# Kernel tuning notes

Measured on AMD Instinct MI355X. Metric: run time of the kernel, lower is better.

The kernel has to match this reference:

```python
import jax, jax.numpy as jnp
import numpy as np

B, G, CE, D, L, H, DH, M, KQ = 4, 64, 384, 512, 8, 16, 32, 2048, 16
NJ, NB = 163, 11
DET_THRESH = 0.3
PATCH = 14.0
EPS = 1e-8


def _ln(x, g, b):
    mu = x.mean(-1, keepdims=True)
    v = x.var(-1, keepdims=True)
    return (x - mu) * jax.lax.rsqrt(v + 1e-5) * g + b


def setup_inputs():
    key = jax.random.key(0)
    ks = iter(jax.random.split(key, 64))
    def n(sh, s=0.02):
        return (jax.random.normal(next(ks), sh) * s).astype(jnp.float32)
    inp = {}
    inp['feat'] = jax.random.normal(next(ks), (B, G, G, CE), dtype=jnp.float32)
    inp['scores'] = jax.random.uniform(next(ks), (B, G, G), dtype=jnp.float32)
    inp['K_cam'] = jnp.tile(jnp.array([[1000., 0., 448.], [0., 1000., 448.], [0., 0., 1.]], dtype=jnp.float32), (B, 1, 1))
    inp['pos_emb'] = n((G * G, D), 1.0)
    inp['Wtok'] = n((CE, D)); inp['btok'] = jnp.zeros((D,), jnp.float32)
    for nm in ['Wq', 'Wk', 'Wv', 'Wo']:
        inp[nm] = n((L, D, D))
    inp['g1'] = jnp.ones((L, D), jnp.float32); inp['b1n'] = jnp.zeros((L, D), jnp.float32)
    inp['W1'] = n((L, D, M)); inp['bf1'] = jnp.zeros((L, M), jnp.float32)
    inp['W2'] = n((L, M, D)); inp['bf2'] = jnp.zeros((L, D), jnp.float32)
    inp['g2'] = jnp.ones((L, D), jnp.float32); inp['b2n'] = jnp.zeros((L, D), jnp.float32)
    inp['offW1'] = n((D, D)); inp['offb1'] = jnp.zeros((D,), jnp.float32)
    inp['offW2'] = n((D, 2)); inp['offb2'] = jnp.zeros((2,), jnp.float32)
    inp['dW1'] = n((D, D)); inp['db1'] = jnp.zeros((D,), jnp.float32)
    inp['dW2'] = n((D, 1)); inp['db2'] = jnp.zeros((1,), jnp.float32)
    inp['sW1'] = n((D, D)); inp['sb1'] = jnp.zeros((D,), jnp.float32)
    inp['sW2'] = n((D, NB)); inp['sb2'] = jnp.zeros((NB,), jnp.float32)
    inp['pW1'] = n((D + NJ * 6, D)); inp['pb1'] = jnp.zeros((D,), jnp.float32)
    inp['pW2'] = n((D, NJ * 6)); inp['pb2'] = jnp.zeros((NJ * 6,), jnp.float32)
    # identity-like 6D init pose per joint: eye(3)[:, :2].flatten() = [1,0,0,1,0,0]
    inp['init_body_pose'] = jnp.tile(jnp.array([1., 0., 0., 1., 0., 0.], dtype=jnp.float32), NJ)
    inp['useful_rotmat'] = (jax.random.uniform(next(ks), (NJ,)) < 0.66).astype(jnp.float32)
    return inp


def reference(feat, scores, K_cam, pos_emb, Wtok, btok,
              Wq, Wk, Wv, Wo, g1, b1n, W1, bf1, W2, bf2, g2, b2n,
              offW1, offb1, offW2, offb2, dW1, db1, dW2, db2,
              sW1, sb1, sW2, sb2, pW1, pb1, pW2, pb2,
              init_body_pose, useful_rotmat):
    # --- NMS via 3x3 max-pool (stride 1, same padding) + threshold ---
    sm = jax.lax.reduce_window(scores, -jnp.inf, jax.lax.max, (1, 3, 3), (1, 1, 1), 'SAME')
    sc = scores * (sm == scores).astype(scores.dtype)
    flat = sc.reshape(B, G * G)
    vals, idx = jax.lax.top_k(flat, KQ)                 # padded ragged detections
    mask = (vals >= DET_THRESH).astype(feat.dtype)      # [B,KQ] validity mask
    row = idx // G
    col = idx % G
    # --- token projection + 2d pos emb, gather queries ---
    dec_emb = feat @ Wtok + btok + pos_emb.reshape(G, G, D)        # [B,G,G,D]
    ctx = dec_emb.reshape(B, G * G, D)                              # context per image
    q = jnp.take_along_axis(ctx, idx[..., None], axis=1)            # [B,KQ,D]
    x = q * mask[..., None]
    scale = DH ** -0.5
    # --- HPH decoder: depth x (prenorm cross-attn to full-image context + FFN) ---
    for l in range(L):
        h = _ln(x, g1[l], b1n[l])
        qh = (h @ Wq[l]).reshape(B, KQ, H, DH)
        kh = (ctx @ Wk[l]).reshape(B, G * G, H, DH)
        vh = (ctx @ Wv[l]).reshape(B, G * G, H, DH)
        att = jax.nn.softmax(jnp.einsum('bqhd,bkhd->bhqk', qh, kh) * scale, axis=-1)
        o = jnp.einsum('bhqk,bkhd->bqhd', att, vh).reshape(B, KQ, H * DH) @ Wo[l]
        x = x + o * mask[..., None]
        h2 = _ln(x, g2[l], b2n[l])
        x = x + (jax.nn.gelu(h2 @ W1[l] + bf1[l]) @ W2[l] + bf2[l]) * mask[..., None]
    y = x.reshape(B * KQ, D)
    m = mask.reshape(B * KQ, 1)
    # --- heads ---
    offset = jax.nn.relu(y @ offW1 + offb1) @ offW2 + offb2          # [N,2]
    loc_coarse = jnp.stack([col.reshape(-1), row.reshape(-1)], -1).astype(y.dtype)
    loc = (loc_coarse + 0.5 + offset) * PATCH
    Kd = jnp.repeat(K_cam, KQ, axis=0)                               # [N,3,3]
    focal = Kd[:, 0, 0]
    d_raw = jax.nn.relu(y @ dW1 + db1) @ dW2 + db2                   # [N,1]
    dist = focal[:, None] / jnp.clip(jnp.exp(d_raw), 1e-5)
    homo = jnp.concatenate([loc, jnp.ones_like(loc[:, :1])], -1)     # [N,3]
    Kinv = jnp.linalg.inv(Kd)
    transl = jnp.einsum('nij,nj->ni', Kinv, homo) * dist             # [N,3]
    shape_ = jax.nn.sigmoid(jax.nn.relu(y @ sW1 + sb1) @ sW2 + sb2)  # [N,11]
    ibp = jnp.broadcast_to(init_body_pose, (B * KQ, NJ * 6))
    rot6d = jax.nn.relu(jnp.concatenate([y, ibp], -1) @ pW1 + pb1) @ pW2 + pb2 + ibp
    # --- special Gram-Schmidt: 6D -> rotation matrices ---
    Mm = rot6d.reshape(-1, NJ, 3, 2)
    u0 = Mm[..., 0]
    u0 = u0 / (jnp.linalg.norm(u0, axis=-1, keepdims=True) + EPS)
    v1 = Mm[..., 1] - jnp.sum(Mm[..., 1] * u0, -1, keepdims=True) * u0
    u1 = v1 / (jnp.linalg.norm(v1, axis=-1, keepdims=True) + EPS)
    u2 = jnp.cross(u0, u1)
    rotmat = jnp.stack([u0, u1, u2], -1)                             # [N,NJ,3,3]
    eye = jnp.eye(3, dtype=rotmat.dtype)
    um = useful_rotmat.reshape(1, NJ, 1, 1)
    rotmat = um * rotmat + (1.0 - um) * eye
    out = jnp.concatenate([loc, offset, dist, transl, shape_, rotmat.reshape(B * KQ, NJ * 9)], -1) * m
    return out
```

## Files before the change

### kernel.cpp

```cpp
#include <hip/hip_runtime.h>

typedef unsigned int uint;
typedef unsigned short u16;

#define BB 4
#define CE 384
#define DD 512
#define LL 8
#define HH 16
#define MM 2048
#define NJ 163
#define TOK 4096
#define BKQ 64
#define QH 256
#define OUTW 1486
#define NROT 978
#define QKSCALE 0.17677669529663687f

typedef __attribute__((ext_vector_type(8))) short short8;
typedef __attribute__((ext_vector_type(4))) float float4v;

static __device__ __forceinline__ u16 f2bf(float f){
  union { float f; uint u; } c; c.f = f;
  uint u = c.u;
  return (u16)((u + 0x7FFFu + ((u >> 16) & 1u)) >> 16);
}
static __device__ __forceinline__ float bf2f(u16 u){
  union { uint u; float f; } c; c.u = ((uint)u) << 16;
  return c.f;
}
static __device__ __forceinline__ float wred_sum(float v){
  for (int o = 32; o; o >>= 1) v += __shfl_xor(v, o, 64);
  return v;
}
static __device__ __forceinline__ void gl16(const void* g, void* l){
  __builtin_amdgcn_global_load_lds((const __attribute__((address_space(1))) void*)g,
                                   (__attribute__((address_space(3))) void*)l, 16, 0, 0);
}

__global__ __launch_bounds__(256) void k_nms_topk(const float* __restrict__ scores,
    int* __restrict__ oidx, float* __restrict__ omask, float* __restrict__ ocol, float* __restrict__ orow)
{
  int b = blockIdx.x, t = threadIdx.x;
  __shared__ float sraw[4096];
  __shared__ float sv[4]; __shared__ int si[4]; __shared__ int swin;
  const float* sp = scores + (size_t)b * 4096;
  for (int i = t; i < 4096; i += 256) sraw[i] = sp[i];
  __syncthreads();
  float v[16];
  #pragma unroll
  for (int j = 0; j < 16; j++){
    int i = t + j*256;
    int r = i >> 6, c = i & 63;
    float mx = -1e30f;
    for (int dr = -1; dr <= 1; dr++){
      int rr = r + dr; if (rr < 0 || rr > 63) continue;
      for (int dc = -1; dc <= 1; dc++){
        int cc = c + dc; if (cc < 0 || cc > 63) continue;
        mx = fmaxf(mx, sraw[rr*64+cc]);
      }
    }
    float s = sraw[i];
    v[j] = (s == mx) ? s : 0.0f;
  }
  int lane = t & 63, wv = t >> 6;
  for (int iter = 0; iter < 16; iter++){
    float best = -1e30f; int bi_ = 1 << 30;
    #pragma unroll
    for (int j = 0; j < 16; j++){
      if (v[j] > best){ best = v[j]; bi_ = t + j*256; }
    }
    #pragma unroll
    for (int o = 32; o; o >>= 1){
      float ov = __shfl_xor(best, o, 64);
      int oi = __shfl_xor(bi_, o, 64);
      if (ov > best || (ov == best && oi < bi_)){ best = ov; bi_ = oi; }
    }
    if (lane == 0){ sv[wv] = best; si[wv] = bi_; }
    __syncthreads();
    if (t == 0){
      float bb = sv[0]; int ii = si[0];
      for (int k = 1; k < 4; k++){
        if (sv[k] > bb || (sv[k] == bb && si[k] < ii)){ bb = sv[k]; ii = si[k]; }
      }
      oidx[b*16+iter] = ii;
      omask[b*16+iter] = (bb >= 0.3f) ? 1.f : 0.f;
      ocol[b*16+iter] = (float)(ii & 63);
      orow[b*16+iter] = (float)(ii >> 6);
      swin = ii;
    }
    __syncthreads();
    int wi = swin;
    if ((wi & 255) == t) v[wi >> 8] = -1e30f;
    __syncthreads();
  }
}

__global__ __launch_bounds__(256) void k_cvt_bf16(const float* __restrict__ in, u16* __restrict__ out, int n4){
  int i = blockIdx.x*256 + threadIdx.x;
  int stride = gridDim.x*256;
  for (int j = i; j < n4; j += stride){
    float4 v = ((const float4*)in)[j];
    ushort4 o;
    o.x = f2bf(v.x); o.y = f2bf(v.y); o.z = f2bf(v.z); o.w = f2bf(v.w);
    ((ushort4*)out)[j] = o;
  }
}

struct PJobs {
  const float* s[24]; u16* d[24];
  int R[24], C[24], t0[25];
  int njobs, ntiles;
};
__global__ __launch_bounds__(256) void k_prep_all(PJobs J,
    const float* __restrict__ pW1, const float* __restrict__ pb1,
    const float* __restrict__ ibp, float* __restrict__ hb4,
    const float* __restrict__ offb1, const float* __restrict__ db1, const float* __restrict__ sb1,
    const float* __restrict__ pb2, float* __restrict__ cvec2)
{
  int bid = blockIdx.x, t = threadIdx.x;
  if (bid < 128){
    int d = bid*4 + (t >> 6);
    int ln = t & 63;
    float acc = 0.f;
    for (int i = ln; i < NJ*6; i += 64) acc += ibp[i] * pW1[(size_t)(DD+i)*DD + d];
    acc = wred_sum(acc);
    if (ln == 0) hb4[1536 + d] = acc + pb1[d];
  } else if (bid == 128){
    for (int i = t; i < 1536; i += 256)
      hb4[i] = (i < 512) ? offb1[i] : (i < 1024 ? db1[i-512] : sb1[i-1024]);
    for (int i = t; i < 1024; i += 256)
      cvec2[i] = (i < NJ*6) ? (pb2[i] + ibp[i]) : 0.f;
  }
  __shared__ float tile[32][33];
  for (int g = bid; g < J.ntiles; g += gridDim.x){
    int j = 0;
    while (g >= J.t0[j+1]) j++;
    int ti = g - J.t0[j];
    int C_ = J.C[j], R_ = J.R[j];
    int tC = (C_ + 31) >> 5;
    int ry = ti / tC, cx = ti - ry*tC;
    int c0 = cx*32, r0 = ry*32;
    int tx = t & 31, ty = t >> 5;
    const float* src = J.s[j]; u16* dst = J.d[j];
    for (int i = 0; i < 32; i += 8){
      float v = 0.f;
      if (c0+tx < C_) v = src[(size_t)(r0+ty+i)*C_ + c0+tx];
      tile[ty+i][tx] = v;
    }
    __syncthreads();
    for (int i = 0; i < 32; i += 8){
      if (c0+ty+i < C_) dst[(size_t)(c0+ty+i)*R_ + r0+tx] = f2bf(tile[tx][ty+i]);
    }
    __syncthreads();
  }
}

__global__ __launch_bounds__(256) void k_wqkvo(const float* __restrict__ wq, const float* __restrict__ wk,
    const float* __restrict__ wv, const float* __restrict__ wo,
    u16* __restrict__ AT, u16* __restrict__ WVOT)
{
  __shared__ __align__(16) u16 As[2560];
  __shared__ __align__(16) u16 Bs[2560];
  int t = threadIdx.x;
  int lane = t & 63, w = t >> 6, lr = lane & 15, lk = lane >> 4;
  float4v acc[4];
  float4v z4 = {0.f,0.f,0.f,0.f};
  acc[0]=z4; acc[1]=z4; acc[2]=z4; acc[3]=z4;
  if (blockIdx.x < 1024){
    int id = blockIdx.x;
    int rt = id & 127, dt = id >> 7;
    int h = rt >> 3, dout0 = (rt & 7)*64, din0 = dt*64;
    int r = t >> 2, c0 = (t & 3)*8;
    {
      float4 u0 = *(const float4*)(wk + (size_t)(dout0+r)*DD + h*32 + c0);
      float4 u1 = *(const float4*)(wk + (size_t)(dout0+r)*DD + h*32 + c0 + 4);
      u16* d = As + r*40 + c0;
      d[0]=f2bf(u0.x); d[1]=f2bf(u0.y); d[2]=f2bf(u0.z); d[3]=f2bf(u0.w);
      d[4]=f2bf(u1.x); d[5]=f2bf(u1.y); d[6]=f2bf(u1.z); d[7]=f2bf(u1.w);
      float4 v0 = *(const float4*)(wq + (size_t)(din0+r)*DD + h*32 + c0);
      float4 v1 = *(const float4*)(wq + (size_t)(din0+r)*DD + h*32 + c0 + 4);
      u16* e = Bs + r*40 + c0;
      e[0]=f2bf(v0.x); e[1]=f2bf(v0.y); e[2]=f2bf(v0.z); e[3]=f2bf(v0.w);
      e[4]=f2bf(v1.x); e[5]=f2bf(v1.y); e[6]=f2bf(v1.z); e[7]=f2bf(v1.w);
    }
    __syncthreads();
    short8 af = *(const short8*)&As[(w*16+lr)*40 + lk*8];
    #pragma unroll
    for (int nf = 0; nf < 4; nf++){
      short8 bf8 = *(const short8*)&Bs[(nf*16+lr)*40 + lk*8];
      acc[nf] = __builtin_amdgcn_mfma_f32_16x16x32_bf16(af, bf8, acc[nf], 0, 0, 0);
    }
    #pragma unroll
    for (int nf = 0; nf < 4; nf++){
      #pragma unroll
      for (int jj = 0; jj < 4; jj++){
        int row = w*16 + lk*4 + jj;
        AT[(size_t)(h*512 + dout0 + row)*DD + din0 + nf*16 + lr] = f2bf(acc[nf][jj]*QKSCALE);
      }
    }
  } else {
    int id = blockIdx.x - 1024;
    int ct = id & 127, dt = id >> 7;
    int h = ct >> 3, Dc0 = (ct & 7)*64, dout0 = dt*64;
    {
      int c = t >> 3, d8 = (t & 7)*8;
      float4 a0 = *(const float4*)(wo + (size_t)(h*32+c)*DD + dout0 + d8);
      float4 a1 = *(const float4*)(wo + (size_t)(h*32+c)*DD + dout0 + d8 + 4);
      As[(d8+0)*40 + c] = f2bf(a0.x);
      As[(d8+1)*40 + c] = f2bf(a0.y);
      As[(d8+2)*40 + c] = f2bf(a0.z);
      As[(d8+3)*40 + c] = f2bf(a0.w);
      As[(d8+4)*40 + c] = f2bf(a1.x);
      As[(d8+5)*40 + c] = f2bf(a1.y);
      As[(d8+6)*40 + c] = f2bf(a1.z);
      As[(d8+7)*40 + c] = f2bf(a1.w);
      int r = t >> 2, c0 = (t & 3)*8;
      float4 v0 = *(const float4*)(wv + (size_t)(Dc0+r)*DD + h*32 + c0);
      float4 v1 = *(const float4*)(wv + (size_t)(Dc0+r)*DD + h*32 + c0 + 4);
      u16* e = Bs + r*40 + c0;
      e[0]=f2bf(v0.x); e[1]=f2bf(v0.y); e[2]=f2bf(v0.z); e[3]=f2bf(v0.w);
      e[4]=f2bf(v1.x); e[5]=f2bf(v1.y); e[6]=f2bf(v1.z); e[7]=f2bf(v1.w);
    }
    __syncthreads();
    short8 af = *(const short8*)&As[(w*16+lr)*40 + lk*8];
    #pragma unroll
    for (int nf = 0; nf < 4; nf++){
      short8 bf8 = *(const short8*)&Bs[(nf*16+lr)*40 + lk*8];
      acc[nf] = __builtin_amdgcn_mfma_f32_16x16x32_bf16(af, bf8, acc[nf], 0, 0, 0);
    }
    #pragma unroll
    for (int nf = 0; nf < 4; nf++){
      #pragma unroll
      for (int jj = 0; jj < 4; jj++){
        int row = w*16 + lk*4 + jj;
        WVOT[(size_t)(dout0 + row)*8192 + h*512 + Dc0 + nf*16 + lr] = f2bf(acc[nf][jj]);
      }
    }
  }
}

__global__ __launch_bounds__(256) void k_red8(const u16* __restrict__ parts, u16* __restrict__ cf){
  int i4 = blockIdx.x*256 + threadIdx.x;
  int elem = i4*4;
  int row = elem >> 13, col = elem & 8191;
  int b = row >> 4, q = row & 15, h = col >> 9, Dc = col & 511;
  const u16* src = parts + ((size_t)b*8)*131072 + (size_t)(q*16+h)*512 + Dc;
  float s0 = 0.f, s1 = 0.f, s2 = 0.f, s3 = 0.f;
  #pragma unroll
  for (int ks = 0; ks < 8; ks++){
    ushort4 g = *(const ushort4*)(src + (size_t)ks*131072);
    s0 += bf2f(g.x); s1 += bf2f(g.y); s2 += bf2f(g.z); s3 += bf2f(g.w);
  }
  ushort4 o;
  o.x = f2bf(s0); o.y = f2bf(s1); o.z = f2bf(s2); o.w = f2bf(s3);
  *(ushort4*)&cf[(size_t)row*8192 + col] = o;
}

__global__ __launch_bounds__(256) void k_gemm_emb(
    const float* __restrict__ feat, const u16* __restrict__ Bt,
    u16* __restrict__ ctx, u16* __restrict__ ctxT,
    const float* __restrict__ ep1, const float* __restrict__ ep2)
{
  __shared__ __align__(16) u16 SM[16640];
  u16* As = SM;
  u16* Bs = SM + 8192;
  int m0 = blockIdx.y*128, n0 = blockIdx.x*128;
  int t = threadIdx.x, lane = t & 63, wave = t >> 6;
  int wr = wave >> 1, wc = wave & 1;
  int lr = lane & 15, lk = lane >> 4;
  int sr8 = t >> 3, sl = t & 7;
  int sw = ((sl ^ (sr8 & 7)) * 8);
  float4v acc[4][4];
  float4v z4 = {0.f, 0.f, 0.f, 0.f};
  #pragma unroll
  for (int i = 0; i < 4; i++)
    #pragma unroll
    for (int j = 0; j < 4; j++) acc[i][j] = z4;
  for (int kt = 0; kt < CE; kt += 64){
    __syncthreads();
    #pragma unroll
    for (int p = 0; p < 8; p++){
      int r = (t >> 4) + p*16, f4 = t & 15;
      float4 v = *(const float4*)&feat[(size_t)(m0+r)*CE + kt + f4*4];
      int dc = ((f4 >> 1) ^ (r & 7))*8 + (f4 & 1)*4;
      ushort4 o; o.x = f2bf(v.x); o.y = f2bf(v.y); o.z = f2bf(v.z); o.w = f2bf(v.w);
      *(ushort4*)&As[r*64 + dc] = o;
    }
    #pragma unroll
    for (int rg = 0; rg < 4; rg++)
      gl16(Bt + (size_t)(n0 + rg*32 + sr8)*CE + kt + sw, Bs + rg*2048 + 8*t);
    __syncthreads();
    #pragma unroll
    for (int s = 0; s < 2; s++){
      int slot = ((s*4 + lk) ^ (lr & 7)) * 8;
      short8 af[4], bfr[4];
      #pragma unroll
      for (int i = 0; i < 4; i++) af[i] = *(const short8*)&As[(wr*64 + i*16 + lr)*64 + slot];
      #pragma unroll
      for (int j = 0; j < 4; j++) bfr[j] = *(const short8*)&Bs[(wc*64 + j*16 + lr)*64 + slot];
      #pragma unroll
      for (int i = 0; i < 4; i++)
        #pragma unroll
        for (int j = 0; j < 4; j++)
          acc[i][j] = __builtin_amdgcn_mfma_f32_16x16x32_bf16(af[i], bfr[j], acc[i][j], 0, 0, 0);
    }
  }
  __syncthreads();
  #pragma unroll
  for (int i = 0; i < 4; i++){
    int rbase = m0 + wr*64 + i*16 + lk*4;
    #pragma unroll
    for (int j = 0; j < 4; j++){
      int cc = n0 + wc*64 + j*16 + lr;
      #pragma unroll
      for (int jj = 0; jj < 4; jj++){
        int rr = rbase + jj;
        float vv = acc[i][j][jj] + ep1[cc] + ep2[(size_t)(rr & 4095)*DD + cc];
        u16 bv = f2bf(vv);
        ctx[(size_t)rr*DD + cc] = bv;
        SM[(cc - n0)*130 + (rr - m0)] = bv;
      }
    }
  }
  __syncthreads();
  int b = m0 >> 12, tok0 = m0 & 4095;
  int tx = t & 63, ty = t >> 6;
  #pragma unroll 4
  for (int it = 0; it < 32; it++){
    int c = ty*32 + it;
    uint vv = *(const uint*)&SM[c*130 + tx*2];
    *(uint*)&ctxT[((size_t)b*DD + n0 + c)*TOK + tok0 + tx*2] = vv;
  }
}

__global__ __launch_bounds__(256) void k_gather2(const u16* __restrict__ ctx, const int* __restrict__ oidx,
    float* __restrict__ x)
{
  int bq = blockIdx.x, t = threadIdx.x;
  int b = bq >> 4, tok = oidx[bq];
  uint v = ((const uint*)(ctx + ((size_t)b*TOK + tok)*DD))[t];
  float2 o; o.x = bf2f((u16)(v & 0xFFFF)); o.y = bf2f((u16)(v >> 16));
  *(float2*)&x[(size_t)bq*DD + t*2] = o;
}

template<int EPI>
__global__ __launch_bounds__(256) void k_gemm_bt64(
    const u16* __restrict__ A, const u16* __restrict__ Bt,
    float* __restrict__ C, u16* __restrict__ Cb,
    int Kslice, int lda, int ldb, int ldc,
    long sA, long sB, long sC, int ksplit)
{
  int bz = blockIdx.z;
  int batch = bz / ksplit, ks = bz - batch*ksplit;
  const u16* Ab = A + (size_t)batch*sA + (size_t)ks*Kslice;
  const u16* Bb = Bt + (size_t)batch*sB + (size_t)ks*Kslice;
  int m0 = blockIdx.y*128, n0 = blockIdx.x*64;
  __shared__ __align__(16) u16 As[128*64];
  __shared__ __align__(16) u16 Bs[64*64];
  int t = threadIdx.x, lane = t & 63, w = t >> 6;
  int lr = lane & 15, lk = lane >> 4;
  int sr8 = t >> 3, sl = t & 7;
  int sw = ((sl ^ (sr8 & 7)) * 8);
  float4v acc[2][4];
  float4v z4 = {0.f,0.f,0.f,0.f};
  #pragma unroll
  for (int i = 0; i < 2; i++)
    #pragma unroll
    for (int j = 0; j < 4; j++) acc[i][j] = z4;

  for (int kt = 0; kt < Kslice; kt += 64){
    __syncthreads();
    #pragma unroll
    for (int rg = 0; rg < 4; rg++)
      gl16(Ab + (size_t)(m0 + rg*32 + sr8)*lda + kt + sw, As + rg*2048 + 8*t);
    #pragma unroll
    for (int rg = 0; rg < 2; rg++)
      gl16(Bb + (size_t)(n0 + rg*32 + sr8)*ldb + kt + sw, Bs + rg*2048 + 8*t);
    __syncthreads();
    #pragma unroll
    for (int s = 0; s < 2; s++){
      int slot = ((s*4 + lk) ^ (lr & 7)) * 8;
      short8 af[2], bfr[4];
      #pragma unroll
      for (int i = 0; i < 2; i++) af[i] = *(const short8*)&As[(w*32 + i*16 + lr)*64 + slot];
      #pragma unroll
      for (int j = 0; j < 4; j++) bfr[j] = *(const short8*)&Bs[(j*16 + lr)*64 + slot];
      #pragma unroll
      for (int i = 0; i < 2; i++)
        #pragma unroll
        for (int j = 0; j < 4; j++)
          acc[i][j] = __builtin_amdgcn_mfma_f32_16x16x32_bf16(af[i], bfr[j], acc[i][j], 0, 0, 0);
    }
  }
  #pragma unroll
  for (int i = 0; i < 2; i++){
    int rbase = m0 + w*32 + i*16 + lk*4;
    #pragma unroll
    for (int j = 0; j < 4; j++){
      int cc = n0 + j*16 + lr;
      #pragma unroll
      for (int jj = 0; jj < 4; jj++){
        int rr = rbase + jj;
        if (EPI == 0) C[(size_t)bz*sC + (size_t)rr*ldc + cc] = acc[i][j][jj];
        else if (EPI == 1) Cb[(size_t)batch*sC + (size_t)rr*ldc + cc] = f2bf(acc[i][j][jj]);
        else Cb[(size_t)bz*sC + (size_t)rr*ldc + cc] = f2bf(acc[i][j][jj]);
      }
    }
  }
}

template<int ACT, int RES, int OUTB, int DOLN, int NG, int HPB, int ZMAP = 0>
__global__ __launch_bounds__(256) void k_mf64(
    const u16* __restrict__ A, const float* __restrict__ xf,
    const float* __restrict__ g, const float* __restrict__ bb,
    const u16* __restrict__ Bt, const float* __restrict__ bias,
    float* __restrict__ C, u16* __restrict__ Cb, u16* __restrict__ Cb2,
    int N, int K, int kper, int ldc, float alpha)
{
  __shared__ __align__(16) u16 Asl[DOLN ? 64*520 : 64*64];
  __shared__ __align__(16) u16 Bs[64*64];
  int t = threadIdx.x, lane = t & 63, w = t >> 6;
  int lr = lane & 15, lk = lane >> 4;
  int n0 = blockIdx.x*64;
  int ks = blockIdx.y, kbeg = ks*kper;
  int sr8 = t >> 3, sl = t & 7;
  int sw = ((sl ^ (sr8 & 7)) * 8);

  if (DOLN){
    for (int rr = 0; rr < 16; rr++){
      int row = w*16 + rr;
      const float* xr = xf + (size_t)row*DD;
      float4 v0 = *(const float4*)(xr + lane*4);
      float4 v1 = *(const float4*)(xr + 256 + lane*4);
      float s = v0.x+v0.y+v0.z+v0.w + v1.x+v1.y+v1.z+v1.w;
      s = wred_sum(s);
      float mu = s * (1.f/DD);
      float d0=v0.x-mu, d1=v0.y-mu, d2=v0.z-mu, d3=v0.w-mu;
      float e0=v1.x-mu, e1=v1.y-mu, e2=v1.z-mu, e3=v1.w-mu;
      float q = d0*d0+d1*d1+d2*d2+d3*d3 + e0*e0+e1*e1+e2*e2+e3*e3;
      q = wred_sum(q);
      float inv = rsqrtf(q * (1.f/DD) + 1e-5f);
      float4 g0 = *(const float4*)(g + lane*4);
      float4 g1 = *(const float4*)(g + 256 + lane*4);
      float4 b0 = *(const float4*)(bb + lane*4);
      float4 b1 = *(const float4*)(bb + 256 + lane*4);
      u16* dst = &Asl[row*520];
      dst[lane*4+0] = f2bf(d0*inv*g0.x + b0.x);
      dst[lane*4+1] = f2bf(d1*inv*g0.y + b0.y);
      dst[lane*4+2] = f2bf(d2*inv*g0.z + b0.z);
      dst[lane*4+3] = f2bf(d3*inv*g0.w + b0.w);
      dst[256+lane*4+0] = f2bf(e0*inv*g1.x + b1.x);
      dst[256+lane*4+1] = f2bf(e1*inv*g1.y + b1.y);
      dst[256+lane*4+2] = f2bf(e2*inv*g1.z + b1.z);
      dst[256+lane*4+3] = f2bf(e3*inv*g1.w + b1.w);
    }
  }

  float4v acc[4];
  float4v z4 = {0.f,0.f,0.f,0.f};
  acc[0]=z4; acc[1]=z4; acc[2]=z4; acc[3]=z4;

  for (int kc = kbeg; kc < kbeg + kper; kc += 64){
    __syncthreads();
    if (!DOLN){
      gl16(A + (size_t)sr8*K + kc + sw,        (u16*)Asl + 8*t);
      gl16(A + (size_t)(32+sr8)*K + kc + sw,   (u16*)Asl + 2048 + 8*t);
    }
    gl16(Bt + (size_t)(n0+sr8)*K + kc + sw,      (u16*)Bs + 8*t);
    gl16(Bt + (size_t)(n0+32+sr8)*K + kc + sw,   (u16*)Bs + 2048 + 8*t);
    __syncthreads();
    #pragma unroll
    for (int s = 0; s < 2; s++){
      int slot = ((s*4 + lk) ^ (lr & 7)) * 8;
      short8 af;
      if (DOLN) af = *(const short8*)&Asl[(w*16+lr)*520 + kc + s*32 + lk*8];
      else      af = *(const short8*)&Asl[(w*16+lr)*64 + slot];
      #pragma unroll
      for (int nf = 0; nf < 4; nf++){
        short8 bf8 = *(const short8*)&Bs[(nf*16+lr)*64 + slot];
        acc[nf] = __builtin_amdgcn_mfma_f32_16x16x32_bf16(af, bf8, acc[nf], 0, 0, 0);
      }
    }
  }
  #pragma unroll
  for (int nf = 0; nf < 4; nf++){
    int col = n0 + nf*16 + lr;
    float bsv = (bias && ks == 0) ? bias[col] : 0.f;
    #pragma unroll
    for (int jj = 0; jj < 4; jj++){
      int row = w*16 + lk*4 + jj;
      float v = acc[nf][jj]*alpha + bsv;
      if (ACT == 1) v = fmaxf(v, 0.f);
      else if (ACT == 2) v = 0.5f*v*(1.f + tanhf(0.7978845608028654f*(v + 0.044715f*v*v*v)));
      if (NG && col >= N) continue;
      if (ZMAP){
        int b_ = row >> 4, q_ = row & 15, h_ = col >> 9, d_ = col & 511;
        Cb[((size_t)b_*QH + (q_ << 4) + h_)*DD + d_] = f2bf(v);
        continue;
      }
      size_t o = (size_t)row*ldc + col;
      if (OUTB == 1) Cb[o] = f2bf(v);
      else if (RES == 0) C[o] = v;
      else atomicAdd(&C[o], v);
      if (HPB && col >= 1536) Cb2[(size_t)row*DD + (col - 1536)] = f2bf(v);
    }
  }
}

__global__ __launch_bounds__(256) void k_softmax(const u16* __restrict__ lg, u16* __restrict__ att){
  int row = blockIdx.x, t = threadIdx.x;
  const uint* p = (const uint*)(lg + (size_t)row*TOK);
  uint pv[8]; float v0[8], v1[8]; float mx = -1e30f;
  #pragma unroll
  for (int i = 0; i < 8; i++){
    pv[i] = p[t + i*256];
    v0[i] = bf2f((u16)(pv[i] & 0xFFFF));
    v1[i] = bf2f((u16)(pv[i] >> 16));
    mx = fmaxf(mx, fmaxf(v0[i], v1[i]));
  }
  int lane = t & 63, w = t >> 6;
  for (int o = 32; o; o >>= 1) mx = fmaxf(mx, __shfl_xor(mx, o, 64));
  __shared__ float sm[4]; __shared__ float ssum[4];
  if (lane == 0) sm[w] = mx;
  __syncthreads();
  mx = fmaxf(fmaxf(sm[0], sm[1]), fmaxf(sm[2], sm[3]));
  float s = 0.f;
  #pragma unroll
  for (int i = 0; i < 8; i++){
    v0[i] = expf(v0[i] - mx); v1[i] = expf(v1[i] - mx);
    s += v0[i] + v1[i];
  }
  s = wred_sum(s);
  if (lane == 0) ssum[w] = s;
  __syncthreads();
  s = ssum[0]+ssum[1]+ssum[2]+ssum[3];
  float inv = 1.f / s;
  uint* q = (uint*)(att + (size_t)row*TOK);
  #pragma unroll
  for (int i = 0; i < 8; i++){
    uint lo = f2bf(v0[i]*inv);
    uint hi = f2bf(v1[i]*inv);
    q[t + i*256] = lo | (hi << 16);
  }
}

__global__ __launch_bounds__(256) void k_final(
    const float* __restrict__ h4, const float* __restrict__ rot6d,
    const float* __restrict__ offW2, const float* __restrict__ offb2,
    const float* __restrict__ dW2, const float* __restrict__ db2,
    const float* __restrict__ sW2, const float* __restrict__ sb2,
    const float* __restrict__ K_cam, const float* __restrict__ useful,
    const float* __restrict__ maskf, const float* __restrict__ colf, const float* __restrict__ rowf,
    float* __restrict__ out)
{
  int bq = blockIdx.x, t = threadIdx.x, b = bq >> 4;
  float po0 = 0.f, po1 = 0.f, pd = 0.f, ps[11];
  #pragma unroll
  for (int j = 0; j < 11; j++) ps[j] = 0.f;
  const float* hrow = h4 + (size_t)bq*2048;
  for (int i = t; i < DD; i += 256){
    float ho = hrow[i];
    float hd = hrow[512 + i];
    float hs = hrow[1024 + i];
    po0 += ho*offW2[i*2]; po1 += ho*offW2[i*2+1];
    pd += hd*dW2[i];
    #pragma unroll
    for (int j = 0; j < 11; j++) ps[j] += hs*sW2[i*11+j];
  }
  __shared__ float sred[4][14];
  __shared__ float sout[14];
  int wv = t >> 6, ln = t & 63;
  float vals[14];
  vals[0] = po0; vals[1] = po1; vals[2] = pd;
  #pragma unroll
  for (int j = 0; j < 11; j++) vals[3+j] = ps[j];
  #pragma unroll
  for (int kk = 0; kk < 14; kk++){
    float r = wred_sum(vals[kk]);
    if (ln == 0) sred[wv][kk] = r;
  }
  __syncthreads();
  if (t < 14) sout[t] = sred[0][t]+sred[1][t]+sred[2][t]+sred[3][t];
  __syncthreads();
  float m = maskf[bq];
  if (t == 0){
    float off0 = sout[0] + offb2[0], off1 = sout[1] + offb2[1];
    float draw = sout[2] + db2[0];
    float l0 = (colf[bq] + 0.5f + off0) * 14.0f;
    float l1 = (rowf[bq] + 0.5f + off1) * 14.0f;
    float fx = K_cam[b*9+0], cx = K_cam[b*9+2], fy = K_cam[b*9+4], cy = K_cam[b*9+5];
    float dist = fx / fmaxf(expf(draw), 1e-5f);
    float tx = (l0 - cx) / fx * dist, ty = (l1 - cy) / fy * dist;
    float* o = out + (size_t)bq*OUTW;
    o[0] = l0*m; o[1] = l1*m; o[2] = off0*m; o[3] = off1*m; o[4] = dist*m;
    o[5] = tx*m; o[6] = ty*m; o[7] = dist*m;
    #pragma unroll
    for (int j = 0; j < 11; j++){ float sp = sout[3+j] + sb2[j]; o[8+j] = m / (1.f + expf(-sp)); }
  }
  if (t < NJ){
    const float* rp = rot6d + (size_t)bq*NROT + t*6;
    float a0 = rp[0], b0 = rp[1], a1 = rp[2], b1 = rp[3], a2 = rp[4], b2 = rp[5];
    float n0 = sqrtf(a0*a0 + a1*a1 + a2*a2);
    float i0 = 1.f / (n0 + 1e-8f);
    float u00 = a0*i0, u01 = a1*i0, u02 = a2*i0;
    float dt = b0*u00 + b1*u01 + b2*u02;
    float v0 = b0 - dt*u00, v1 = b1 - dt*u01, v2 = b2 - dt*u02;
    float n1 = sqrtf(v0*v0 + v1*v1 + v2*v2);
    float i1 = 1.f / (n1 + 1e-8f);
    float u10 = v0*i1, u11 = v1*i1, u12 = v2*i1;
    float u20 = u01*u12 - u02*u11;
    float u21 = u02*u10 - u00*u12;
    float u22 = u00*u11 - u01*u10;
    float um = useful[t], om = 1.f - um;
    float R00 = um*u00 + om, R01 = um*u10,      R02 = um*u20;
    float R10 = um*u01,      R11 = um*u11 + om, R12 = um*u21;
    float R20 = um*u02,      R21 = um*u12,      R22 = um*u22 + om;
    float* o = out + (size_t)bq*OUTW + 19 + t*9;
    o[0] = R00*m; o[1] = R01*m; o[2] = R02*m;
    o[3] = R10*m; o[4] = R11*m; o[5] = R12*m;
    o[6] = R20*m; o[7] = R21*m; o[8] = R22*m;
  }
}

extern "C" void kernel_launch(void* const* d_in, const int* in_sizes, int n_in,
                              void* d_out, int out_size, void* d_ws, size_t ws_size,
                              hipStream_t stream)
{
  const float* feat   = (const float*)d_in[0];
  const float* scores = (const float*)d_in[1];
  const float* K_cam  = (const float*)d_in[2];
  const float* pos_emb= (const float*)d_in[3];
  const float* Wtok   = (const float*)d_in[4];
  const float* btok   = (const float*)d_in[5];
  const float* Wq     = (const float*)d_in[6];
  const float* Wk     = (const float*)d_in[7];
  const float* Wv     = (const float*)d_in[8];
  const float* Wo     = (const float*)d_in[9];
  const float* g1     = (const float*)d_in[10];
  const float* b1n    = (const float*)d_in[11];
  const float* W1     = (const float*)d_in[12];
  const float* bf1    = (const float*)d_in[13];
  const float* W2     = (const float*)d_in[14];
  const float* bf2    = (const float*)d_in[15];
  const float* g2     = (const float*)d_in[16];
  const float* b2n    = (const float*)d_in[17];
  const float* offW1  = (const float*)d_in[18];
  const float* offb1  = (const float*)d_in[19];
  const float* offW2  = (const float*)d_in[20];
  const float* offb2  = (const float*)d_in[21];
  const float* dW1    = (const float*)d_in[22];
  const float* db1    = (const float*)d_in[23];
  const float* dW2    = (const float*)d_in[24];
  const float* db2    = (const float*)d_in[25];
  const float* sW1    = (const float*)d_in[26];
  const float* sb1    = (const float*)d_in[27];
  const float* sW2    = (const float*)d_in[28];
  const float* sb2    = (const float*)d_in[29];
  const float* pW1    = (const float*)d_in[30];
  const float* pb1    = (const float*)d_in[31];
  const float* pW2    = (const float*)d_in[32];
  const float* pb2    = (const float*)d_in[33];
  const float* ibp    = (const float*)d_in[34];
  const float* useful = (const float*)d_in[35];
  float* out = (float*)d_out;

  char* wsp = (char*)d_ws;
  size_t off = 0;
  auto alloc = [&](size_t bytes)->char*{
    char* p = wsp + off;
    off += (bytes + 255) & ~((size_t)255);
    return p;
  };
  int*   t_idx  = (int*)  alloc(BKQ*4);
  float* t_mask = (float*)alloc(BKQ*4);
  float* t_col  = (float*)alloc(BKQ*4);
  float* t_row  = (float*)alloc(BKQ*4);
  u16*   wtokT  = (u16*)  alloc((size_t)DD*CE*2);
  u16*   ctx_bf = (u16*)  alloc((size_t)BB*TOK*DD*2);
  u16*   ctxT_bf= (u16*)  alloc((size_t)BB*TOK*DD*2);
  u16*   ATb    = (u16*)  alloc((size_t)8192*DD*2);
  u16*   WVOb   = (u16*)  alloc((size_t)DD*8192*2);
  u16*   w1T    = (u16*)  alloc((size_t)LL*DD*MM*2);
  u16*   w2T    = (u16*)  alloc((size_t)LL*MM*DD*2);
  u16*   headsT = (u16*)  alloc((size_t)4*DD*DD*2);
  u16*   pw2T   = (u16*)  alloc((size_t)1024*DD*2);
  float* x      = (float*)alloc((size_t)BKQ*DD*4);
  u16*   x_bf   = (u16*)  alloc((size_t)BKQ*DD*2);
  u16*   z_bf   = (u16*)  alloc((size_t)BKQ*HH*DD*2);
  u16*   logits = (u16*)  alloc((size_t)BB*QH*TOK*2);
  u16*   att_bf = (u16*)  alloc((size_t)BB*QH*TOK*2);
  u16*   parts  = (u16*)  alloc((size_t)BB*8*QH*DD*2);
  u16*   c_flat = (u16*)  alloc((size_t)BKQ*8192*2);
  u16*   mid_bf = (u16*)  alloc((size_t)BKQ*MM*2);
  float* h4     = (float*)alloc((size_t)BKQ*2048*4);
  u16*   hp_bf  = (u16*)  alloc((size_t)BKQ*DD*2);
  float* hb4    = (float*)alloc(2048*4);
  float* cvec2  = (float*)alloc(1024*4);
  float* rot6d  = (float*)alloc((size_t)BKQ*NROT*4);
  if (off > ws_size) return;

  PJobs J;
  int ntl = 0, nj = 0;
  auto addjob = [&](const float* s, u16* d, int R, int C){
    J.s[nj] = s; J.d[nj] = d; J.R[nj] = R; J.C[nj] = C; J.t0[nj] = ntl;
    ntl += ((R+31)/32) * ((C+31)/32);
    nj++;
  };
  addjob(Wtok, wtokT, CE, DD);
  for (int l = 0; l < LL; l++) addjob(W1 + (size_t)l*DD*MM, w1T + (size_t)l*MM*DD, DD, MM);
  for (int l = 0; l < LL; l++) addjob(W2 + (size_t)l*MM*DD, w2T + (size_t)l*DD*MM, MM, DD);
  addjob(offW1, headsT,            DD, DD);
  addjob(dW1,   headsT + DD*DD,    DD, DD);
  addjob(sW1,   headsT + 2*DD*DD,  DD, DD);
  addjob(pW1,   headsT + 3*DD*DD,  DD, DD);
  addjob(pW2,   pw2T, DD, NROT);
  J.t0[nj] = ntl; J.njobs = nj; J.ntiles = ntl;

  k_nms_topk<<<BB, 256, 0, stream>>>(scores, t_idx, t_mask, t_col, t_row);
  k_prep_all<<<2048, 256, 0, stream>>>(J, pW1, pb1, ibp, hb4, offb1, db1, sb1, pb2, cvec2);
  k_gemm_emb<<<dim3(DD/128, (BB*TOK)/128, 1), 256, 0, stream>>>(feat, wtokT, ctx_bf, ctxT_bf, btok, pos_emb);
  k_gather2<<<BKQ, 256, 0, stream>>>(ctx_bf, t_idx, x);

  for (int l = 0; l < LL; l++){
    k_wqkvo<<<2048, 256, 0, stream>>>(Wq + (size_t)l*DD*DD, Wk + (size_t)l*DD*DD,
                                      Wv + (size_t)l*DD*DD, Wo + (size_t)l*DD*DD, ATb, WVOb);
    k_mf64<0,0,0,1,0,0,1><<<dim3(128,1), 256, 0, stream>>>(
        nullptr, x, g1 + l*DD, b1n + l*DD, ATb, nullptr,
        nullptr, z_bf, nullptr, 8192, DD, DD, DD, 1.f);
    k_gemm_bt64<1><<<dim3(TOK/64, 2, BB), 256, 0, stream>>>(
        z_bf, ctx_bf, nullptr, logits,
        DD, DD, DD, TOK, (long)QH*DD, (long)TOK*DD, (long)QH*TOK, 1);
    k_softmax<<<BB*QH, 256, 0, stream>>>(logits, att_bf);
    k_gemm_bt64<2><<<dim3(DD/64, 2, BB*8), 256, 0, stream>>>(
        att_bf, ctxT_bf, nullptr, parts,
        TOK/8, TOK, TOK, DD, (long)QH*TOK, (long)DD*TOK, (long)QH*DD, 8);
    k_red8<<<512, 256, 0, stream>>>(parts, c_flat);
    k_mf64<0,1,0,0,0,0,0><<<dim3(8,16), 256, 0, stream>>>(
        c_flat, nullptr, nullptr, nullptr, WVOb, nullptr,
        x, nullptr, nullptr, DD, 8192, 512, DD, 1.f);
    k_mf64<2,0,1,1,0,0,0><<<dim3(MM/64,1), 256, 0, stream>>>(
        nullptr, x, g2 + l*DD, b2n + l*DD, w1T + (size_t)l*DD*MM, bf1 + l*MM,
        nullptr, mid_bf, nullptr, MM, DD, DD, MM, 1.f);
    k_mf64<0,1,0,0,0,0,0><<<dim3(8,8), 256, 0, stream>>>(
        mid_bf, nullptr, nullptr, nullptr, w2T + (size_t)l*MM*DD, bf2 + l*DD,
        x, nullptr, nullptr, DD, MM, MM/8, DD, 1.f);
  }

  k_cvt_bf16<<<32, 256, 0, stream>>>(x, x_bf, BKQ*DD/4);
  k_mf64<1,0,0,0,0,1,0><<<dim3(32,1), 256, 0, stream>>>(
      x_bf, nullptr, nullptr, nullptr, headsT, hb4,
      h4, nullptr, hp_bf, 2048, DD, DD, 2048, 1.f);
  k_mf64<0,0,0,0,1,0,0><<<dim3(16,1), 256, 0, stream>>>(
      hp_bf, nullptr, nullptr, nullptr, pw2T, cvec2,
      rot6d, nullptr, nullptr, NROT, DD, DD, NROT, 1.f);
  k_final<<<BKQ, 256, 0, stream>>>(h4, rot6d, offW2, offb2, dW2, db2, sW2, sb2,
                                   K_cam, useful, t_mask, t_col, t_row, out);
}
```

Baseline: 911.4 us.

## Batch per-layer QKVO weight prep into one launch and fuse small kernels

Moves the NMS/top-k selection into the prep kernel's first four blocks and hoists the per-layer Wq/Wk/Wv/Wo folding out of the layer loop into one 16384-block launch that writes all layers' folded weights up front. The transpose tiles in prep now cover 64 rows and store packed bf16 pairs. The final bf16 conversion of x is folded into the head GEMM's load path through a new DOLN==2 mode. This removes several launches and serial per-layer weight work from the loop, at the cost of eight times more workspace for the folded weights.

```diff
diff --git a/kernel.cpp b/kernel.cpp
--- a/kernel.cpp
+++ b/kernel.cpp
@@ -38,101 +38,90 @@
                                    (__attribute__((address_space(3))) void*)l, 16, 0, 0);
 }
 
-__global__ __launch_bounds__(256) void k_nms_topk(const float* __restrict__ scores,
-    int* __restrict__ oidx, float* __restrict__ omask, float* __restrict__ ocol, float* __restrict__ orow)
-{
-  int b = blockIdx.x, t = threadIdx.x;
-  __shared__ float sraw[4096];
-  __shared__ float sv[4]; __shared__ int si[4]; __shared__ int swin;
-  const float* sp = scores + (size_t)b * 4096;
-  for (int i = t; i < 4096; i += 256) sraw[i] = sp[i];
-  __syncthreads();
-  float v[16];
-  #pragma unroll
-  for (int j = 0; j < 16; j++){
-    int i = t + j*256;
-    int r = i >> 6, c = i & 63;
-    float mx = -1e30f;
-    for (int dr = -1; dr <= 1; dr++){
-      int rr = r + dr; if (rr < 0 || rr > 63) continue;
-      for (int dc = -1; dc <= 1; dc++){
-        int cc = c + dc; if (cc < 0 || cc > 63) continue;
-        mx = fmaxf(mx, sraw[rr*64+cc]);
-      }
-    }
-    float s = sraw[i];
-    v[j] = (s == mx) ? s : 0.0f;
-  }
-  int lane = t & 63, wv = t >> 6;
-  for (int iter = 0; iter < 16; iter++){
-    float best = -1e30f; int bi_ = 1 << 30;
-    #pragma unroll
-    for (int j = 0; j < 16; j++){
-      if (v[j] > best){ best = v[j]; bi_ = t + j*256; }
-    }
-    #pragma unroll
-    for (int o = 32; o; o >>= 1){
-      float ov = __shfl_xor(best, o, 64);
-      int oi = __shfl_xor(bi_, o, 64);
-      if (ov > best || (ov == best && oi < bi_)){ best = ov; bi_ = oi; }
-    }
-    if (lane == 0){ sv[wv] = best; si[wv] = bi_; }
-    __syncthreads();
-    if (t == 0){
-      float bb = sv[0]; int ii = si[0];
-      for (int k = 1; k < 4; k++){
-        if (sv[k] > bb || (sv[k] == bb && si[k] < ii)){ bb = sv[k]; ii = si[k]; }
-      }
-      oidx[b*16+iter] = ii;
-      omask[b*16+iter] = (bb >= 0.3f) ? 1.f : 0.f;
-      ocol[b*16+iter] = (float)(ii & 63);
-      orow[b*16+iter] = (float)(ii >> 6);
-      swin = ii;
-    }
-    __syncthreads();
-    int wi = swin;
-    if ((wi & 255) == t) v[wi >> 8] = -1e30f;
-    __syncthreads();
-  }
-}
-
-__global__ __launch_bounds__(256) void k_cvt_bf16(const float* __restrict__ in, u16* __restrict__ out, int n4){
-  int i = blockIdx.x*256 + threadIdx.x;
-  int stride = gridDim.x*256;
-  for (int j = i; j < n4; j += stride){
-    float4 v = ((const float4*)in)[j];
-    ushort4 o;
-    o.x = f2bf(v.x); o.y = f2bf(v.y); o.z = f2bf(v.z); o.w = f2bf(v.w);
-    ((ushort4*)out)[j] = o;
-  }
-}
-
 struct PJobs {
   const float* s[24]; u16* d[24];
   int R[24], C[24], t0[25];
   int njobs, ntiles;
 };
 __global__ __launch_bounds__(256) void k_prep_all(PJobs J,
+    const float* __restrict__ scores,
+    int* __restrict__ oidx, float* __restrict__ omask, float* __restrict__ ocol, float* __restrict__ orow,
     const float* __restrict__ pW1, const float* __restrict__ pb1,
     const float* __restrict__ ibp, float* __restrict__ hb4,
     const float* __restrict__ offb1, const float* __restrict__ db1, const float* __restrict__ sb1,
     const float* __restrict__ pb2, float* __restrict__ cvec2)
 {
   int bid = blockIdx.x, t = threadIdx.x;
-  if (bid < 128){
-    int d = bid*4 + (t >> 6);
+  __shared__ float sraw[4096];
+  __shared__ float sv[4]; __shared__ int si[4]; __shared__ int swin;
+  __shared__ u16 tb[32][66];
+
+  if (bid < 4){
+    int b = bid;
+    const float* sp = scores + (size_t)b * 4096;
+    for (int i = t; i < 4096; i += 256) sraw[i] = sp[i];
+    __syncthreads();
+    float v[16];
+    #pragma unroll
+    for (int j = 0; j < 16; j++){
+      int i = t + j*256;
+      int r = i >> 6, c = i & 63;
+      float mx = -1e30f;
+      for (int dr = -1; dr <= 1; dr++){
+        int rr = r + dr; if (rr < 0 || rr > 63) continue;
+        for (int dc = -1; dc <= 1; dc++){
+          int cc = c + dc; if (cc < 0 || cc > 63) continue;
+          mx = fmaxf(mx, sraw[rr*64+cc]);
+        }
+      }
+      float s = sraw[i];
+      v[j] = (s == mx) ? s : 0.0f;
+    }
+    int lane = t & 63, wv = t >> 6;
+    for (int iter = 0; iter < 16; iter++){
+      float best = -1e30f; int bi_ = 1 << 30;
+      #pragma unroll
+      for (int j = 0; j < 16; j++){
+        if (v[j] > best){ best = v[j]; bi_ = t + j*256; }
+      }
+      #pragma unroll
+      for (int o = 32; o; o >>= 1){
+        float ov = __shfl_xor(best, o, 64);
+        int oi = __shfl_xor(bi_, o, 64);
+        if (ov > best || (ov == best && oi < bi_)){ best = ov; bi_ = oi; }
+      }
+      if (lane == 0){ sv[wv] = best; si[wv] = bi_; }
+      __syncthreads();
+      if (t == 0){
+        float bb = sv[0]; int ii = si[0];
+        for (int k = 1; k < 4; k++){
+          if (sv[k] > bb || (sv[k] == bb && si[k] < ii)){ bb = sv[k]; ii = si[k]; }
+        }
+        oidx[b*16+iter] = ii;
+        omask[b*16+iter] = (bb >= 0.3f) ? 1.f : 0.f;
+        ocol[b*16+iter] = (float)(ii & 63);
+        orow[b*16+iter] = (float)(ii >> 6);
+        swin = ii;
+      }
+      __syncthreads();
+      int wi = swin;
+      if ((wi & 255) == t) v[wi >> 8] = -1e30f;
+      __syncthreads();
+    }
+  } else if (bid < 132){
+    int d = (bid - 4)*4 + (t >> 6);
     int ln = t & 63;
     float acc = 0.f;
     for (int i = ln; i < NJ*6; i += 64) acc += ibp[i] * pW1[(size_t)(DD+i)*DD + d];
     acc = wred_sum(acc);
     if (ln == 0) hb4[1536 + d] = acc + pb1[d];
-  } else if (bid == 128){
+  } else if (bid == 132){
     for (int i = t; i < 1536; i += 256)
       hb4[i] = (i < 512) ? offb1[i] : (i < 1024 ? db1[i-512] : sb1[i-1024]);
     for (int i = t; i < 1024; i += 256)
       cvec2[i] = (i < NJ*6) ? (pb2[i] + ibp[i]) : 0.f;
   }
-  __shared__ float tile[32][33];
+
   for (int g = bid; g < J.ntiles; g += gridDim.x){
     int j = 0;
     while (g >= J.t0[j+1]) j++;
@@ -140,35 +129,51 @@
     int C_ = J.C[j], R_ = J.R[j];
     int tC = (C_ + 31) >> 5;
     int ry = ti / tC, cx = ti - ry*tC;
-    int c0 = cx*32, r0 = ry*32;
+    int r0 = ry*64, c0 = cx*32;
     int tx = t & 31, ty = t >> 5;
     const float* src = J.s[j]; u16* dst = J.d[j];
-    for (int i = 0; i < 32; i += 8){
+    __syncthreads();
+    #pragma unroll
+    for (int i = 0; i < 8; i++){
+      int r = ty + i*8;
       float v = 0.f;
-      if (c0+tx < C_) v = src[(size_t)(r0+ty+i)*C_ + c0+tx];
-      tile[ty+i][tx] = v;
-    }
-    __syncthreads();
-    for (int i = 0; i < 32; i += 8){
-      if (c0+ty+i < C_) dst[(size_t)(c0+ty+i)*R_ + r0+tx] = f2bf(tile[tx][ty+i]);
-    }
-    __syncthreads();
-  }
-}
-
-__global__ __launch_bounds__(256) void k_wqkvo(const float* __restrict__ wq, const float* __restrict__ wk,
-    const float* __restrict__ wv, const float* __restrict__ wo,
-    u16* __restrict__ AT, u16* __restrict__ WVOT)
+      if (c0+tx < C_) v = src[(size_t)(r0+r)*C_ + c0+tx];
+      tb[tx][r] = f2bf(v);
+    }
+    __syncthreads();
+    #pragma unroll
+    for (int p = 0; p < 4; p++){
+      int c = (t >> 5) + p*8;
+      int rr = t & 31;
+      if (c0 + c < C_){
+        uint val = (uint)tb[c][2*rr] | ((uint)tb[c][2*rr+1] << 16);
+        *(uint*)&dst[(size_t)(c0+c)*R_ + r0 + rr*2] = val;
+      }
+    }
+  }
+}
+
+__global__ __launch_bounds__(256) void k_wqkvo_all(const float* __restrict__ Wq, const float* __restrict__ Wk,
+    const float* __restrict__ Wv, const float* __restrict__ Wo,
+    u16* __restrict__ ATall, u16* __restrict__ WVOall)
 {
   __shared__ __align__(16) u16 As[2560];
   __shared__ __align__(16) u16 Bs[2560];
   int t = threadIdx.x;
+  int l = blockIdx.x >> 11;
+  int bid = blockIdx.x & 2047;
+  const float* wq = Wq + (size_t)l*DD*DD;
+  const float* wk = Wk + (size_t)l*DD*DD;
+  const float* wv = Wv + (size_t)l*DD*DD;
+  const float* wo = Wo + (size_t)l*DD*DD;
+  u16* AT  = ATall  + (size_t)l*8192*DD;
+  u16* WVOT= WVOall + (size_t)l*DD*8192;
   int lane = t & 63, w = t >> 6, lr = lane & 15, lk = lane >> 4;
   float4v acc[4];
   float4v z4 = {0.f,0.f,0.f,0.f};
   acc[0]=z4; acc[1]=z4; acc[2]=z4; acc[3]=z4;
-  if (blockIdx.x < 1024){
-    int id = blockIdx.x;
+  if (bid < 1024){
+    int id = bid;
     int rt = id & 127, dt = id >> 7;
     int h = rt >> 3, dout0 = (rt & 7)*64, din0 = dt*64;
     int r = t >> 2, c0 = (t & 3)*8;
@@ -200,7 +205,7 @@
       }
     }
   } else {
-    int id = blockIdx.x - 1024;
+    int id = bid - 1024;
     int ct = id & 127, dt = id >> 7;
     int h = ct >> 3, Dc0 = (ct & 7)*64, dout0 = dt*64;
     {
@@ -427,7 +432,7 @@
   int sr8 = t >> 3, sl = t & 7;
   int sw = ((sl ^ (sr8 & 7)) * 8);
 
-  if (DOLN){
+  if (DOLN == 1){
     for (int rr = 0; rr < 16; rr++){
       int row = w*16 + rr;
       const float* xr = xf + (size_t)row*DD;
@@ -454,6 +459,22 @@
       dst[256+lane*4+1] = f2bf(e1*inv*g1.y + b1.y);
       dst[256+lane*4+2] = f2bf(e2*inv*g1.z + b1.z);
       dst[256+lane*4+3] = f2bf(e3*inv*g1.w + b1.w);
+    }
+  } else if (DOLN == 2){
+    for (int rr = 0; rr < 16; rr++){
+      int row = w*16 + rr;
+      const float* xr = xf + (size_t)row*DD;
+      float4 v0 = *(const float4*)(xr + lane*4);
+      float4 v1 = *(const float4*)(xr + 256 + lane*4);
+      u16* dst = &Asl[row*520];
+      dst[lane*4+0] = f2bf(v0.x);
+      dst[lane*4+1] = f2bf(v0.y);
+      dst[lane*4+2] = f2bf(v0.z);
+      dst[lane*4+3] = f2bf(v0.w);
+      dst[256+lane*4+0] = f2bf(v1.x);
+      dst[256+lane*4+1] = f2bf(v1.y);
+      dst[256+lane*4+2] = f2bf(v1.z);
+      dst[256+lane*4+3] = f2bf(v1.w);
     }
   }
 
@@ -679,14 +700,13 @@
   u16*   wtokT  = (u16*)  alloc((size_t)DD*CE*2);
   u16*   ctx_bf = (u16*)  alloc((size_t)BB*TOK*DD*2);
   u16*   ctxT_bf= (u16*)  alloc((size_t)BB*TOK*DD*2);
-  u16*   ATb    = (u16*)  alloc((size_t)8192*DD*2);
-  u16*   WVOb   = (u16*)  alloc((size_t)DD*8192*2);
+  u16*   ATall  = (u16*)  alloc((size_t)LL*8192*DD*2);
+  u16*   WVOall = (u16*)  alloc((size_t)LL*DD*8192*2);
   u16*   w1T    = (u16*)  alloc((size_t)LL*DD*MM*2);
   u16*   w2T    = (u16*)  alloc((size_t)LL*MM*DD*2);
   u16*   headsT = (u16*)  alloc((size_t)4*DD*DD*2);
   u16*   pw2T   = (u16*)  alloc((size_t)1024*DD*2);
   float* x      = (float*)alloc((size_t)BKQ*DD*4);
-  u16*   x_bf   = (u16*)  alloc((size_t)BKQ*DD*2);
   u16*   z_bf   = (u16*)  alloc((size_t)BKQ*HH*DD*2);
   u16*   logits = (u16*)  alloc((size_t)BB*QH*TOK*2);
   u16*   att_bf = (u16*)  alloc((size_t)BB*QH*TOK*2);
@@ -704,7 +724,7 @@
   int ntl = 0, nj = 0;
   auto addjob = [&](const float* s, u16* d, int R, int C){
     J.s[nj] = s; J.d[nj] = d; J.R[nj] = R; J.C[nj] = C; J.t0[nj] = ntl;
-    ntl += ((R+31)/32) * ((C+31)/32);
+    ntl += (R/64) * ((C+31)/32);
     nj++;
   };
   addjob(Wtok, wtokT, CE, DD);
@@ -717,16 +737,15 @@
   addjob(pW2,   pw2T, DD, NROT);
   J.t0[nj] = ntl; J.njobs = nj; J.ntiles = ntl;
 
-  k_nms_topk<<<BB, 256, 0, stream>>>(scores, t_idx, t_mask, t_col, t_row);
-  k_prep_all<<<2048, 256, 0, stream>>>(J, pW1, pb1, ibp, hb4, offb1, db1, sb1, pb2, cvec2);
+  k_prep_all<<<2048, 256, 0, stream>>>(J, scores, t_idx, t_mask, t_col, t_row,
+                                       pW1, pb1, ibp, hb4, offb1, db1, sb1, pb2, cvec2);
+  k_wqkvo_all<<<16384, 256, 0, stream>>>(Wq, Wk, Wv, Wo, ATall, WVOall);
   k_gemm_emb<<<dim3(DD/128, (BB*TOK)/128, 1), 256, 0, stream>>>(feat, wtokT, ctx_bf, ctxT_bf, btok, pos_emb);
   k_gather2<<<BKQ, 256, 0, stream>>>(ctx_bf, t_idx, x);
 
   for (int l = 0; l < LL; l++){
-    k_wqkvo<<<2048, 256, 0, stream>>>(Wq + (size_t)l*DD*DD, Wk + (size_t)l*DD*DD,
-                                      Wv + (size_t)l*DD*DD, Wo + (size_t)l*DD*DD, ATb, WVOb);
     k_mf64<0,0,0,1,0,0,1><<<dim3(128,1), 256, 0, stream>>>(
-        nullptr, x, g1 + l*DD, b1n + l*DD, ATb, nullptr,
+        nullptr, x, g1 + l*DD, b1n + l*DD, ATall + (size_t)l*8192*DD, nullptr,
         nullptr, z_bf, nullptr, 8192, DD, DD, DD, 1.f);
     k_gemm_bt64<1><<<dim3(TOK/64, 2, BB), 256, 0, stream>>>(
         z_bf, ctx_bf, nullptr, logits,
@@ -737,7 +756,7 @@
         TOK/8, TOK, TOK, DD, (long)QH*TOK, (long)DD*TOK, (long)QH*DD, 8);
     k_red8<<<512, 256, 0, stream>>>(parts, c_flat);
     k_mf64<0,1,0,0,0,0,0><<<dim3(8,16), 256, 0, stream>>>(
-        c_flat, nullptr, nullptr, nullptr, WVOb, nullptr,
+        c_flat, nullptr, nullptr, nullptr, WVOall + (size_t)l*DD*8192, nullptr,
         x, nullptr, nullptr, DD, 8192, 512, DD, 1.f);
     k_mf64<2,0,1,1,0,0,0><<<dim3(MM/64,1), 256, 0, stream>>>(
         nullptr, x, g2 + l*DD, b2n + l*DD, w1T + (size_t)l*DD*MM, bf1 + l*MM,
@@ -747,9 +766,8 @@
         x, nullptr, nullptr, DD, MM, MM/8, DD, 1.f);
   }
 
-  k_cvt_bf16<<<32, 256, 0, stream>>>(x, x_bf, BKQ*DD/4);
-  k_mf64<1,0,0,0,0,1,0><<<dim3(32,1), 256, 0, stream>>>(
-      x_bf, nullptr, nullptr, nullptr, headsT, hb4,
+  k_mf64<1,0,0,2,0,1,0><<<dim3(32,1), 256, 0, stream>>>(
+      nullptr, x, nullptr, nullptr, headsT, hb4,
       h4, nullptr, hp_bf, 2048, DD, DD, 2048, 1.f);
   k_mf64<0,0,0,0,1,0,0><<<dim3(16,1), 256, 0, stream>>>(
       hp_bf, nullptr, nullptr, nullptr, pw2T, cvec2,
```

After: 972.3 us. 1.07x slower.
